# Kernel optimization log

Measured on AMD Instinct MI355X. Metric: run time of the kernel, lower is better.

Reference implementation:

```python
import jax, jax.numpy as jnp
import numpy as np

CHUNK = 32
FLOOR = 0.01
EPS_MIX = 1e-5
EPS_NORM = 1e-5


def l2norm(x):
    return x / jnp.sqrt(jnp.sum(x * x, -1, keepdims=True) + 1e-12)


def dw_causal_conv(x, w):
    # x: (B, L, C), w: (C, K) depthwise causal conv, tap K-1 is 'current'
    K = w.shape[-1]
    L = x.shape[1]
    xp = jnp.pad(x, ((0, 0), (K - 1, 0), (0, 0)))
    y = jnp.zeros_like(x)
    for t in range(K):
        y = y + xp[:, t:t + L, :] * w[:, t]
    return y


def delta_rule_chunkwise(q, k, v, beta):
    # q,k: (B,H,L,dk), v: (B,H,L,dv), beta: (B,H,L); L % CHUNK == 0
    b, h, L, dk = q.shape
    dv = v.shape[-1]
    c = CHUNK
    n = L // c
    q = l2norm(q)
    k = l2norm(k)
    v = v * beta[..., None]
    kb = k * beta[..., None]
    rs = lambda x: x.reshape(b, h, n, c, -1)
    qc, kc, vc, kbc = rs(q), rs(k), rs(v), rs(kb)
    # in-chunk inverse of (I + tril(K_beta K^T)) via forward substitution
    T = -jnp.einsum('bhnid,bhnjd->bhnij', kbc, kc)
    tri_strict = jnp.tril(jnp.ones((c, c), bool), -1)
    T = jnp.where(tri_strict, T, 0.0)
    for i in range(1, c):
        T = T.at[..., i, :i].add(
            jnp.einsum('bhnj,bhnji->bhni', T[..., i, :], T[..., :, :i]))
    T = T + jnp.eye(c, dtype=T.dtype)
    u = jnp.einsum('bhnij,bhnjd->bhnid', T, vc)
    w = jnp.einsum('bhnij,bhnjd->bhnid', T, kbc)
    mask_incl = jnp.tril(jnp.ones((c, c), bool), 0)

    def step(S, inp):
        qi, ki, ui, wi = inp  # each (b,h,c,d)
        attn = jnp.einsum('bhid,bhjd->bhij', qi, ki)
        attn = jnp.where(mask_incl, attn, 0.0)
        u_i = ui - jnp.einsum('bhik,bhkd->bhid', wi, S)
        o_i = jnp.einsum('bhik,bhkd->bhid', qi, S) + jnp.einsum('bhij,bhjd->bhid', attn, u_i)
        S = S + jnp.einsum('bhci,bhcd->bhid', ki, u_i)
        return S, o_i

    S0 = jnp.zeros((b, h, dk, dv), q.dtype)
    xs = tuple(jnp.moveaxis(a, 2, 0) for a in (qc, kc, u, w))
    S, o = jax.lax.scan(step, S0, xs)
    o = jnp.moveaxis(o, 0, 2).reshape(b, h, L, dv)
    return o, S


def setup_inputs() -> dict:
    key = jax.random.key(0)
    B, L, D, H = 4, 4096, 1024, 4
    dh = D // H  # 256
    ks = jax.random.split(key, 20)
    s = 1.0 / np.sqrt(D)
    inp = {
        'hidden_states': jax.random.normal(ks[0], (B, L, D), jnp.float32),
        'Wq': jax.random.normal(ks[1], (D, D), jnp.float32) * s,
        'Wk': jax.random.normal(ks[2], (D, D), jnp.float32) * s,
        'Wv': jax.random.normal(ks[3], (D, D), jnp.float32) * s,
        'Wb': jax.random.normal(ks[4], (D, H), jnp.float32) * s,
        'conv_q_w': jax.random.normal(ks[5], (D, 4), jnp.float32) * 0.5,
        'conv_k_w': jax.random.normal(ks[6], (D, 4), jnp.float32) * 0.5,
        'conv_v_w': jax.random.normal(ks[7], (D, 4), jnp.float32) * 0.5,
        'local_w': (jax.random.normal(ks[8], (H * dh, 7), jnp.float32) / np.sqrt(7.0)).at[:, -1].add(1.0),
        'mid_w': (jax.random.normal(ks[9], (H * dh, 25), jnp.float32) / np.sqrt(25.0)).at[:, -1].add(1.0),
        'r_w1': jax.random.normal(ks[10], (D + 14 * H, 2 * (D + 14 * H)), jnp.float32) / np.sqrt(D + 14 * H),
        'r_b1': jnp.zeros((2 * (D + 14 * H),), jnp.float32),
        'r_w2': jax.random.normal(ks[11], (2 * (D + 14 * H), H * 4), jnp.float32) / np.sqrt(2.0 * (D + 14 * H)),
        'r_b2': jnp.zeros((H, 4), jnp.float32).at[:, 2:].set(0.7).reshape(-1),
        'mix_w': jnp.ones((H, dh), jnp.float32),
        'onorm_w': jnp.ones((dh,), jnp.float32),
        'Wo': jax.random.normal(ks[12], (D, D), jnp.float32) * s,
    }
    return inp


def reference(hidden_states, Wq, Wk, Wv, Wb, conv_q_w, conv_k_w, conv_v_w,
              local_w, mid_w, r_w1, r_b1, r_w2, r_b2, mix_w, onorm_w, Wo):
    B, L, D = hidden_states.shape
    H = mix_w.shape[0]
    dh = mix_w.shape[1]
    # projections + short causal depthwise convs with SiLU (qk_activation='silu')
    q = jax.nn.silu(dw_causal_conv(hidden_states @ Wq, conv_q_w))
    k = jax.nn.silu(dw_causal_conv(hidden_states @ Wk, conv_k_w))
    v = jax.nn.silu(dw_causal_conv(hidden_states @ Wv, conv_v_w))
    q4 = q.reshape(B, L, H, dh)
    k4 = k.reshape(B, L, H, dh)
    v4 = v.reshape(B, L, H, dh)
    beta = jax.nn.sigmoid(hidden_states @ Wb)  # (B,L,H)
    delta_out, _ = delta_rule_chunkwise(
        jnp.transpose(q4, (0, 2, 1, 3)), jnp.transpose(k4, (0, 2, 1, 3)),
        jnp.transpose(v4, (0, 2, 1, 3)), jnp.transpose(beta, (0, 2, 1)))
    delta_out = jnp.transpose(delta_out, (0, 2, 1, 3))  # (B,L,H,dh)
    v_direct = v4
    vflat = v4.reshape(B, L, H * dh)
    local_out = dw_causal_conv(vflat, local_w).reshape(B, L, H, dh)
    mid_out = dw_causal_conv(vflat, mid_w).reshape(B, L, H, dh)
    outs = [local_out, mid_out, delta_out, v_direct]
    # router stats: per-head mean/var of each path + pairwise mean dots
    feats = []
    for o_ in outs:
        feats.append(o_.mean(-1))
        feats.append(jnp.var(o_, -1, ddof=1))
    for i in range(4):
        for j in range(i + 1, 4):
            feats.append((outs[i] * outs[j]).mean(-1))
    router_feat = jnp.concatenate([hidden_states] + feats, axis=-1)  # (B,L,D+14H)
    h1 = jax.nn.silu(router_feat @ r_w1 + r_b1)
    logits = (h1 @ r_w2 + r_b2).reshape(B, L, H, 4)
    p = jax.nn.softmax(logits, -1)
    p = p * (1.0 - 4.0 * FLOOR) + FLOOR  # probability floor
    mixed = sum(p[..., i:i + 1] * outs[i] for i in range(4))  # (B,L,H,dh)
    # MixNorm: per-token per-head RMSNorm with (H,dh) affine
    rms = jnp.sqrt(jnp.mean(mixed * mixed, -1, keepdims=True) + EPS_MIX)
    mixed = mixed / rms * mix_w
    # output RMSNorm (per head_v_dim)
    rms2 = jnp.sqrt(jnp.mean(mixed * mixed, -1, keepdims=True) + EPS_NORM)
    o_n = mixed / rms2 * onorm_w
    return o_n.reshape(B, L, H * dh) @ Wo
```

## Files before the change

### kernel.cpp

```cpp
#include <hip/hip_runtime.h>
#include <cstdint>
#include <cstddef>

typedef unsigned short u16;
typedef __bf16 bf16x8 __attribute__((ext_vector_type(8)));
typedef float    f32x4 __attribute__((ext_vector_type(4)));
typedef unsigned short u16x8 __attribute__((ext_vector_type(8)));
typedef unsigned short u16x4 __attribute__((ext_vector_type(4)));

#define MFMA16(a,b,c) __builtin_amdgcn_mfma_f32_16x16x32_bf16(a,b,c,0,0,0)

__device__ __forceinline__ float bf2f(u16 u){ return __uint_as_float(((unsigned)u)<<16); }
__device__ __forceinline__ u16 f2bf(float f){
  unsigned x = __float_as_uint(f);
  unsigned r = x + 0x7fffu + ((x>>16)&1u);
  return (u16)(r>>16);
}
__device__ __forceinline__ float wred(float v){
  #pragma unroll
  for (int o=32;o;o>>=1) v += __shfl_xor(v,o,64);
  return v;
}
__device__ __forceinline__ float siluf(float x){ return x/(1.f+__expf(-x)); }

__global__ __launch_bounds__(256) void k_zero(float* __restrict__ p, int n){
  int i = blockIdx.x*256 + threadIdx.x;
  if (i < n) p[i] = 0.f;
}

__global__ __launch_bounds__(256) void k_cvt(const float* __restrict__ src,
                                             u16* __restrict__ dst, int n){
  int i = (blockIdx.x*256 + threadIdx.x)*4;
  if (i < n){
    float4 f = *(const float4*)(src + i);
    u16x4 o; o[0]=f2bf(f.x); o[1]=f2bf(f.y); o[2]=f2bf(f.z); o[3]=f2bf(f.w);
    *(u16x4*)(dst + i) = o;
  }
}

__global__ __launch_bounds__(256) void k_tr(const float* __restrict__ src, u16* __restrict__ dst,
                                            int R, int C, int Rp, int Cp){
  __shared__ float t[32][33];
  int n0 = blockIdx.x*32, k0 = blockIdx.y*32;
  int tx = threadIdx.x & 31, ty = threadIdx.x >> 5;
  #pragma unroll
  for (int j=0;j<4;j++){
    int k = k0 + ty + j*8, nn = n0 + tx;
    t[ty + j*8][tx] = (k < R && nn < C) ? src[k*C + nn] : 0.f;
  }
  __syncthreads();
  #pragma unroll
  for (int j=0;j<4;j++){
    int nn = n0 + ty + j*8, k = k0 + tx;
    dst[nn*Rp + k] = f2bf(t[tx][ty + j*8]);
  }
}

__global__ __launch_bounds__(256) void k_pad_w2t(const float* __restrict__ src, u16* __restrict__ dst){
  int k = blockIdx.x*256 + threadIdx.x;
  int j = blockIdx.y;
  if (k < 2176) dst[j*2176 + k] = (k < 2160) ? f2bf(src[k*16 + j]) : (u16)0;
}
__global__ __launch_bounds__(256) void k_pad_b1(const float* __restrict__ src, float* __restrict__ dst){
  int i = blockIdx.x*256 + threadIdx.x;
  if (i < 2176) dst[i] = (i<2160) ? src[i] : 0.f;
}

__global__ __launch_bounds__(256) void k_trk(const u16* __restrict__ kn, u16* __restrict__ kTb){
  __shared__ u16 vs[32][264];
  const int g = blockIdx.x;
  const int bh = g >> 7, nc = g & 127;
  const int b = bh >> 2, h = bh & 3;
  const int tid = threadIdx.x;
  const int rr = tid >> 3, cb = (tid & 7) * 32;
  const u16* src = kn + (size_t)(b*4096 + nc*32 + rr)*1024 + h*256 + cb;
  #pragma unroll
  for (int v=0; v<4; ++v){
    u16x8 x = *(const u16x8*)(src + v*8);
    *(u16x8*)&vs[rr][cb + v*8] = x;
  }
  __syncthreads();
  u16* dst = kTb + ((size_t)g*256 + tid)*32;
  #pragma unroll
  for (int v=0; v<4; ++v){
    u16x8 o;
    #pragma unroll
    for (int e=0; e<8; e++) o[e] = vs[v*8 + e][tid];
    *(u16x8*)(dst + v*8) = o;
  }
}

__global__ __launch_bounds__(256,2) void k_gemm(
    const u16* __restrict__ A, const u16* __restrict__ Bt, void* __restrict__ Cvp,
    int M, int N, int K, int out_f32)
{
  __shared__ u16 As[2][128*64];
  __shared__ u16 Bs[2][128*64];
  const int tid = threadIdx.x;
  const int lane = tid & 63, wv = tid >> 6;
  const int wm = (wv>>1)*64, wn = (wv&1)*64;
  const int r15 = lane & 15, q4 = lane >> 4;
  const int bm0 = blockIdx.y*128, bn0 = blockIdx.x*128;
  const int srow = tid>>3, sch = tid&7;
  const int nk = K >> 6;

  const f32x4 fz = {0.f,0.f,0.f,0.f};
  f32x4 acc[4][4];
  #pragma unroll
  for (int i=0;i<4;i++){
    #pragma unroll
    for (int j=0;j<4;j++) acc[i][j] = fz;
  }

  {
    u16x8 ca[4], cb[4];
    #pragma unroll
    for (int i=0;i<4;i++){
      int r = i*32 + srow;
      ca[i] = *(const u16x8*)(A  + (size_t)(bm0+r)*K + sch*8);
      cb[i] = *(const u16x8*)(Bt + (size_t)(bn0+r)*K + sch*8);
    }
    #pragma unroll
    for (int i=0;i<4;i++){
      int r = i*32 + srow;
      int byt = r*128 + ((sch ^ (r&7))*16);
      *(u16x8*)((char*)(&As[0][0]) + byt) = ca[i];
      *(u16x8*)((char*)(&Bs[0][0]) + byt) = cb[i];
    }
  }
  int cur = 0;
  for (int t=0; t<nk; ++t){
    u16x8 na[4], nb[4];
    if (t+1 < nk){
      const int kt = (t+1)<<6;
      #pragma unroll
      for (int i=0;i<4;i++){
        int r = i*32 + srow;
        na[i] = *(const u16x8*)(A  + (size_t)(bm0+r)*K + kt + sch*8);
        nb[i] = *(const u16x8*)(Bt + (size_t)(bn0+r)*K + kt + sch*8);
      }
    }
    __syncthreads();
    const u16* as_ = &As[cur][0];
    const u16* bs_ = &Bs[cur][0];
    #pragma unroll
    for (int kk=0; kk<2; ++kk){
      bf16x8 av[4], bv[4];
      #pragma unroll
      for (int mi=0;mi<4;mi++){
        int row = wm + mi*16 + r15;
        int ch  = kk*4 + q4;
        av[mi] = *(const bf16x8*)((const char*)as_ + row*128 + ((ch ^ (row&7))*16));
      }
      #pragma unroll
      for (int ni=0;ni<4;ni++){
        int row = wn + ni*16 + r15;
        int ch  = kk*4 + q4;
        bv[ni] = *(const bf16x8*)((const char*)bs_ + row*128 + ((ch ^ (row&7))*16));
      }
      #pragma unroll
      for (int mi=0;mi<4;mi++){
        #pragma unroll
        for (int ni=0;ni<4;ni++)
          acc[mi][ni] = MFMA16(av[mi], bv[ni], acc[mi][ni]);
      }
    }
    if (t+1 < nk){
      #pragma unroll
      for (int i=0;i<4;i++){
        int r = i*32 + srow;
        int byt = r*128 + ((sch ^ (r&7))*16);
        *(u16x8*)((char*)(&As[cur^1][0]) + byt) = na[i];
        *(u16x8*)((char*)(&Bs[cur^1][0]) + byt) = nb[i];
      }
    }
    cur ^= 1;
  }
  float* Cf = (float*)Cvp;
  u16*  Cb2 = (u16*)Cvp;
  #pragma unroll
  for (int mi=0;mi<4;mi++){
    #pragma unroll
    for (int ni=0;ni<4;ni++){
      int gr = bm0 + wm + mi*16 + q4*4;
      int gc = bn0 + wn + ni*16 + r15;
      #pragma unroll
      for (int rg=0; rg<4; ++rg){
        float v = acc[mi][ni][rg];
        size_t off = (size_t)(gr+rg)*N + gc;
        if (out_f32) Cf[off] = v; else Cb2[off] = f2bf(v);
      }
    }
  }
}

union SMu {
  struct { u16 As[2][128*64]; u16 Bs[2][128*64]; } g;
  u16 h1s[128][136];
};
__global__ __launch_bounds__(256,2) void k_gemm_router(
    const u16* __restrict__ A, const u16* __restrict__ Bt,
    const float* __restrict__ bias, const u16* __restrict__ w2t,
    float* __restrict__ logits)
{
  __shared__ SMu sm;
  const int tid = threadIdx.x;
  const int lane = tid & 63, wv = tid >> 6;
  const int wm = (wv>>1)*64, wn = (wv&1)*64;
  const int r15 = lane & 15, q4 = lane >> 4;
  const int bm0 = blockIdx.y*128, bn0 = blockIdx.x*128;
  const int srow = tid>>3, sch = tid&7;
  const int K = 1088, nk = 17;

  const f32x4 fz = {0.f,0.f,0.f,0.f};
  f32x4 acc[4][4];
  #pragma unroll
  for (int i=0;i<4;i++){
    #pragma unroll
    for (int j=0;j<4;j++) acc[i][j] = fz;
  }
  {
    u16x8 ca[4], cb[4];
    #pragma unroll
    for (int i=0;i<4;i++){
      int r = i*32 + srow;
      ca[i] = *(const u16x8*)(A  + (size_t)(bm0+r)*K + sch*8);
      cb[i] = *(const u16x8*)(Bt + (size_t)(bn0+r)*K + sch*8);
    }
    #pragma unroll
    for (int i=0;i<4;i++){
      int r = i*32 + srow;
      int byt = r*128 + ((sch ^ (r&7))*16);
      *(u16x8*)((char*)(&sm.g.As[0][0]) + byt) = ca[i];
      *(u16x8*)((char*)(&sm.g.Bs[0][0]) + byt) = cb[i];
    }
  }
  int cur = 0;
  for (int t=0; t<nk; ++t){
    u16x8 na[4], nb[4];
    if (t+1 < nk){
      const int kt = (t+1)<<6;
      #pragma unroll
      for (int i=0;i<4;i++){
        int r = i*32 + srow;
        na[i] = *(const u16x8*)(A  + (size_t)(bm0+r)*K + kt + sch*8);
        nb[i] = *(const u16x8*)(Bt + (size_t)(bn0+r)*K + kt + sch*8);
      }
    }
    __syncthreads();
    const u16* as_ = &sm.g.As[cur][0];
    const u16* bs_ = &sm.g.Bs[cur][0];
    #pragma unroll
    for (int kk=0; kk<2; ++kk){
      bf16x8 av[4], bv[4];
      #pragma unroll
      for (int mi=0;mi<4;mi++){
        int row = wm + mi*16 + r15;
        int ch  = kk*4 + q4;
        av[mi] = *(const bf16x8*)((const char*)as_ + row*128 + ((ch ^ (row&7))*16));
      }
      #pragma unroll
      for (int ni=0;ni<4;ni++){
        int row = wn + ni*16 + r15;
        int ch  = kk*4 + q4;
        bv[ni] = *(const bf16x8*)((const char*)bs_ + row*128 + ((ch ^ (row&7))*16));
      }
      #pragma unroll
      for (int mi=0;mi<4;mi++){
        #pragma unroll
        for (int ni=0;ni<4;ni++)
          acc[mi][ni] = MFMA16(av[mi], bv[ni], acc[mi][ni]);
      }
    }
    if (t+1 < nk){
      #pragma unroll
      for (int i=0;i<4;i++){
        int r = i*32 + srow;
        int byt = r*128 + ((sch ^ (r&7))*16);
        *(u16x8*)((char*)(&sm.g.As[cur^1][0]) + byt) = na[i];
        *(u16x8*)((char*)(&sm.g.Bs[cur^1][0]) + byt) = nb[i];
      }
    }
    cur ^= 1;
  }
  __syncthreads();
  #pragma unroll
  for (int mi=0;mi<4;mi++){
    #pragma unroll
    for (int ni=0;ni<4;ni++){
      int lr = wm + mi*16 + q4*4;
      int lc = wn + ni*16 + r15;
      float bv_ = bias[bn0 + lc];
      #pragma unroll
      for (int rg=0; rg<4; ++rg)
        sm.h1s[lr+rg][lc] = f2bf(siluf(acc[mi][ni][rg] + bv_));
    }
  }
  __syncthreads();
  f32x4 lacc[2] = {fz, fz};
  #pragma unroll
  for (int rt=0; rt<2; ++rt){
    #pragma unroll
    for (int ks=0; ks<4; ++ks){
      bf16x8 a = *(const bf16x8*)((const char*)&sm.h1s[wv*32 + rt*16 + r15][0] + ks*64 + q4*16);
      bf16x8 b = *(const bf16x8*)(w2t + r15*2176 + bn0 + ks*32 + q4*8);
      lacc[rt] = MFMA16(a, b, lacc[rt]);
    }
  }
  #pragma unroll
  for (int rt=0; rt<2; ++rt){
    #pragma unroll
    for (int rg=0; rg<4; ++rg){
      int m = bm0 + wv*32 + rt*16 + q4*4 + rg;
      atomicAdd(&logits[m*16 + r15], lacc[rt][rg]);
    }
  }
}

__global__ __launch_bounds__(256) void k_softm(float* __restrict__ p, const float* __restrict__ b2){
  int m = blockIdx.x*256 + threadIdx.x;
  float l[16];
  #pragma unroll
  for (int j=0;j<16;j++) l[j] = p[m*16+j] + b2[j];
  #pragma unroll
  for (int hh=0;hh<4;hh++){
    float l0=l[hh*4+0], l1=l[hh*4+1], l2=l[hh*4+2], l3=l[hh*4+3];
    float mx = fmaxf(fmaxf(l0,l1),fmaxf(l2,l3));
    float e0=__expf(l0-mx), e1=__expf(l1-mx), e2=__expf(l2-mx), e3=__expf(l3-mx);
    float iv = 1.f/(e0+e1+e2+e3);
    p[m*16+hh*4+0]=e0*iv*0.96f+0.01f;
    p[m*16+hh*4+1]=e1*iv*0.96f+0.01f;
    p[m*16+hh*4+2]=e2*iv*0.96f+0.01f;
    p[m*16+hh*4+3]=e3*iv*0.96f+0.01f;
  }
}

__global__ __launch_bounds__(256) void k_beta(const u16* __restrict__ Xb,
                                              const float* __restrict__ Wb,
                                              float* __restrict__ beta){
  int m = blockIdx.x*4 + (threadIdx.x>>6);
  int lane = threadIdx.x & 63;
  float a0=0.f,a1=0.f,a2=0.f,a3=0.f;
  #pragma unroll 4
  for (int i=0;i<16;i++){
    int k = lane + i*64;
    float x = bf2f(Xb[m*1024 + k]);
    float4 wr = *(const float4*)(Wb + k*4);
    a0 += x*wr.x; a1 += x*wr.y; a2 += x*wr.z; a3 += x*wr.w;
  }
  a0 = wred(a0); a1 = wred(a1); a2 = wred(a2); a3 = wred(a3);
  if (lane == 0){
    beta[m*4+0] = 1.f/(1.f+__expf(-a0));
    beta[m*4+1] = 1.f/(1.f+__expf(-a1));
    beta[m*4+2] = 1.f/(1.f+__expf(-a2));
    beta[m*4+3] = 1.f/(1.f+__expf(-a3));
  }
}

__global__ __launch_bounds__(256) void k_conv(const u16* __restrict__ raw,
                                              const float* __restrict__ cw,
                                              u16* __restrict__ outp, int do_norm){
  const int m = blockIdx.x;
  const int tid = threadIdx.x, lane = tid&63, hh = tid>>6;
  const int l = m & 4095;
  const int cbase = hh*256 + lane*4;
  float x[4][4];
  #pragma unroll
  for (int j=0;j<4;j++){
    if (l >= j){
      u16x4 xv = *(const u16x4*)(raw + (m-j)*1024 + cbase);
      #pragma unroll
      for (int e=0;e<4;e++) x[j][e] = bf2f(xv[e]);
    } else {
      #pragma unroll
      for (int e=0;e<4;e++) x[j][e] = 0.f;
    }
  }
  float y[4]; float ss = 0.f;
  #pragma unroll
  for (int e=0;e<4;e++){
    int c = cbase + e;
    float yy = x[0][e]*cw[c*4+3] + x[1][e]*cw[c*4+2] + x[2][e]*cw[c*4+1] + x[3][e]*cw[c*4+0];
    yy = siluf(yy);
    y[e] = yy; ss += yy*yy;
  }
  if (do_norm){
    ss = wred(ss);
    float sc = rsqrtf(ss + 1e-12f);
    #pragma unroll
    for (int e=0;e<4;e++) y[e] *= sc;
  }
  u16x4 o;
  #pragma unroll
  for (int e=0;e<4;e++) o[e] = f2bf(y[e]);
  *(u16x4*)(outp + m*1024 + cbase) = o;
}

__global__ __launch_bounds__(256) void k_localmid(const u16* __restrict__ v,
                                                  const float* __restrict__ lw,
                                                  const float* __restrict__ mw,
                                                  u16* __restrict__ lo, u16* __restrict__ mo){
  __shared__ u16 vs[56][256];
  const int lt0 = blockIdx.x*32;
  const int b = blockIdx.y;
  const int c0 = blockIdx.z*256;
  const int tid = threadIdx.x;
  #pragma unroll
  for (int i=0;i<7;i++){
    int flat = tid + i*256;
    int row = flat >> 5;
    int cc = (flat & 31)*8;
    int tok = lt0 - 24 + row;
    u16x8 val = {0,0,0,0,0,0,0,0};
    if (tok >= 0) val = *(const u16x8*)(v + (b*4096 + tok)*1024 + c0 + cc);
    *(u16x8*)&vs[row][cc] = val;
  }
  __syncthreads();
  const int c = tid;
  float lwr[7], mwr[25];
  #pragma unroll
  for (int i=0;i<7;i++) lwr[i] = lw[(c0+c)*7 + i];
  #pragma unroll
  for (int i=0;i<25;i++) mwr[i] = mw[(c0+c)*25 + i];
  for (int lt=0; lt<32; ++lt){
    float a7=0.f, a25=0.f;
    #pragma unroll
    for (int t=0;t<25;t++) a25 += bf2f(vs[lt+t][c]) * mwr[t];
    #pragma unroll
    for (int t=0;t<7;t++)  a7  += bf2f(vs[18+lt+t][c]) * lwr[t];
    int m = b*4096 + lt0 + lt;
    lo[m*1024 + c0 + c] = f2bf(a7);
    mo[m*1024 + c0 + c] = f2bf(a25);
  }
}

__global__ __launch_bounds__(256,2) void k_chunk(
    const u16* __restrict__ qn, const u16* __restrict__ kn, const u16* __restrict__ v,
    const float* __restrict__ beta, u16* __restrict__ u_, u16* __restrict__ w_,
    u16* __restrict__ attnb)
{
  const int chk = blockIdx.x;
  const int nc = chk & 127;
  const int bh = chk >> 7;
  const int b = bh >> 2, h = bh & 3;
  const int tok0 = b*4096 + nc*32;
  const int tid = threadIdx.x, lane = tid&63, wv = tid>>6;
  const int r15 = lane&15, q4 = lane>>4;

  __shared__ u16 kbT[256][40];
  __shared__ u16 vbT[256][40];
  __shared__ float Tm[4][32][33];
  __shared__ u16 Xs[32][40];

  {
    int rr = tid >> 3;
    int cb = (tid & 7)*32;
    float bt = beta[(tok0 + rr)*4 + h];
    const u16* ksrc = kn + (tok0+rr)*1024 + h*256 + cb;
    const u16* vsrc = v  + (tok0+rr)*1024 + h*256 + cb;
    #pragma unroll
    for (int vvv=0; vvv<4; ++vvv){
      u16x8 kx = *(const u16x8*)(ksrc + vvv*8);
      u16x8 vx = *(const u16x8*)(vsrc + vvv*8);
      #pragma unroll
      for (int e=0;e<8;e++){
        kbT[cb + vvv*8 + e][rr] = f2bf(bf2f(kx[e]) * bt);
        vbT[cb + vvv*8 + e][rr] = f2bf(bf2f(vx[e]) * bt);
      }
    }
  }
  {
    const int i0 = (wv>>1)*16, j0 = (wv&1)*16;
    float bi = beta[(tok0 + i0 + r15)*4 + h];
    f32x4 tacc = {0.f,0.f,0.f,0.f};
    #pragma unroll
    for (int ks=0; ks<8; ++ks){
      u16x8 ar = *(const u16x8*)(kn + (tok0 + i0 + r15)*1024 + h*256 + ks*32 + q4*8);
      union { u16x8 u; bf16x8 bf; } au;
      #pragma unroll
      for (int e=0;e<8;e++) au.u[e] = f2bf(bf2f(ar[e]) * bi);
      bf16x8 bv = *(const bf16x8*)(kn + (tok0 + j0 + r15)*1024 + h*256 + ks*32 + q4*8);
      tacc = MFMA16(au.bf, bv, tacc);
    }
    #pragma unroll
    for (int rg=0; rg<4; ++rg){
      int i = i0 + q4*4 + rg, j = j0 + r15;
      float val = (i > j) ? -tacc[rg] : 0.f;
      Tm[0][i][j] = val;
      Tm[2][i][j] = val + ((i==j)?1.f:0.f);
    }
  }
  __syncthreads();
  int cbuf = 0, cx = 2;
  const int ii = tid >> 3, jj = (tid&7)*4;
  for (int s=0; s<4; ++s){
    int nb = cbuf^1, nx = cx^1;
    {
      float o0=0.f,o1=0.f,o2=0.f,o3=0.f;
      for (int k=0;k<32;k++){
        float a = Tm[cbuf][ii][k];
        o0 += a*Tm[cbuf][k][jj+0]; o1 += a*Tm[cbuf][k][jj+1];
        o2 += a*Tm[cbuf][k][jj+2]; o3 += a*Tm[cbuf][k][jj+3];
      }
      Tm[nb][ii][jj+0]=o0; Tm[nb][ii][jj+1]=o1; Tm[nb][ii][jj+2]=o2; Tm[nb][ii][jj+3]=o3;
    }
    __syncthreads();
    {
      float o0=Tm[cx][ii][jj+0], o1=Tm[cx][ii][jj+1], o2=Tm[cx][ii][jj+2], o3=Tm[cx][ii][jj+3];
      for (int k=0;k<32;k++){
        float a = Tm[nb][ii][k];
        o0 += a*Tm[cx][k][jj+0]; o1 += a*Tm[cx][k][jj+1];
        o2 += a*Tm[cx][k][jj+2]; o3 += a*Tm[cx][k][jj+3];
      }
      Tm[nx][ii][jj+0]=o0; Tm[nx][ii][jj+1]=o1; Tm[nx][ii][jj+2]=o2; Tm[nx][ii][jj+3]=o3;
    }
    __syncthreads();
    cbuf = nb; cx = nx;
  }
  {
    #pragma unroll
    for (int e=0;e<4;e++) Xs[ii][jj+e] = f2bf(Tm[cx][ii][jj+e]);
  }
  __syncthreads();
  {
    #pragma unroll
    for (int nt=0; nt<4; ++nt){
      int n0 = wv*64 + nt*16;
      #pragma unroll
      for (int mt=0; mt<2; ++mt){
        bf16x8 a = *(const bf16x8*)((const char*)&Xs[mt*16 + r15][0] + q4*16);
        bf16x8 bu = *(const bf16x8*)((const char*)&vbT[n0 + r15][0] + q4*16);
        bf16x8 bw = *(const bf16x8*)((const char*)&kbT[n0 + r15][0] + q4*16);
        f32x4 ua = {0.f,0.f,0.f,0.f};
        f32x4 wa = {0.f,0.f,0.f,0.f};
        ua = MFMA16(a, bu, ua);
        wa = MFMA16(a, bw, wa);
        #pragma unroll
        for (int rg=0;rg<4;rg++){
          int row = mt*16 + q4*4 + rg;
          int col = n0 + r15;
          u_[(chk*32 + row)*256 + col] = f2bf(ua[rg]);
          w_[(chk*32 + row)*256 + col] = f2bf(wa[rg]);
        }
      }
    }
  }
  {
    const int i0 = (wv>>1)*16, j0 = (wv&1)*16;
    f32x4 aacc = {0.f,0.f,0.f,0.f};
    #pragma unroll
    for (int ks=0;ks<8;++ks){
      bf16x8 a = *(const bf16x8*)(qn + (tok0 + i0 + r15)*1024 + h*256 + ks*32 + q4*8);
      bf16x8 bv = *(const bf16x8*)(kn + (tok0 + j0 + r15)*1024 + h*256 + ks*32 + q4*8);
      aacc = MFMA16(a, bv, aacc);
    }
    #pragma unroll
    for (int rg=0;rg<4;rg++){
      int i = i0 + q4*4 + rg, j = j0 + r15;
      attnb[chk*1024 + i*32 + j] = f2bf((i>=j)? aacc[rg] : 0.f);
    }
  }
}

#define SCAN_BODY(NC, WCUR, WNXT, CB, NB) { \
  const int chk_ = bh*128 + (NC); \
  const int ncn_ = ((NC)+1 < 128) ? (NC)+1 : 127; \
  const int chkn_ = bh*128 + ncn_; \
  u16x8 kst[4]; \
  { const u16* kc = kTb + (size_t)chkn_*8192 + tid*32; \
    _Pragma("unroll") for (int v=0;v<4;++v) kst[v] = *(const u16x8*)(kc + v*8); } \
  _Pragma("unroll") for (int ks=0;ks<8;++ks) \
    WNXT[ks] = *(const u16x8*)(w_ + (size_t)(chkn_*32 + tm*16 + r15)*256 + ks*32 + q4*8); \
  u16x8 qv[8]; \
  _Pragma("unroll") for (int ks=0;ks<8;++ks) \
    qv[ks] = *(const u16x8*)(qn + (size_t)(b*4096 + (NC)*32 + tm*16 + r15)*1024 + h*256 + ks*32 + q4*8); \
  u16x8 atv = *(const u16x8*)(attnb + (size_t)chk_*1024 + (tm*16 + r15)*32 + q4*8); \
  u16 uvv[4]; \
  _Pragma("unroll") for (int rg=0;rg<4;++rg) \
    uvv[rg] = u_[(size_t)(chk_*32 + tm*16 + q4*4 + rg)*256 + dv0 + tn*16 + r15]; \
  f32x4 ua = fz, ub2 = fz; \
  _Pragma("unroll") for (int ks=0;ks<8;ks+=2){ \
    bf16x8 s0 = *(const bf16x8*)((const char*)&Sb[CB][tn*16 + r15][0] + ks*64 + q4*16); \
    ua = MFMA16(*(const bf16x8*)&WCUR[ks], s0, ua); \
    bf16x8 s1 = *(const bf16x8*)((const char*)&Sb[CB][tn*16 + r15][0] + (ks+1)*64 + q4*16); \
    ub2 = MFMA16(*(const bf16x8*)&WCUR[ks+1], s1, ub2); } \
  _Pragma("unroll") for (int rg=0;rg<4;++rg){ \
    float uiv = bf2f(uvv[rg]) - ua[rg] - ub2[rg]; \
    uT[tn*16 + r15][tm*16 + q4*4 + rg] = f2bf(uiv); } \
  __syncthreads(); \
  f32x4 oa = fz, ob = fz; \
  _Pragma("unroll") for (int ks=0;ks<8;ks+=2){ \
    bf16x8 s0 = *(const bf16x8*)((const char*)&Sb[CB][tn*16 + r15][0] + ks*64 + q4*16); \
    oa = MFMA16(*(const bf16x8*)&qv[ks], s0, oa); \
    bf16x8 s1 = *(const bf16x8*)((const char*)&Sb[CB][tn*16 + r15][0] + (ks+1)*64 + q4*16); \
    ob = MFMA16(*(const bf16x8*)&qv[ks+1], s1, ob); } \
  { bf16x8 bu = *(const bf16x8*)((const char*)&uT[tn*16 + r15][0] + q4*16); \
    oa = MFMA16(*(const bf16x8*)&atv, bu, oa); } \
  _Pragma("unroll") for (int rg=0;rg<4;++rg) \
    od[(size_t)(b*4096 + (NC)*32 + tm*16 + q4*4 + rg)*1024 + h*256 + dv0 + tn*16 + r15] = f2bf(oa[rg] + ob[rg]); \
  _Pragma("unroll") for (int mt=0;mt<4;++mt){ \
    bf16x8 a = *(const bf16x8*)((const char*)&knT[CB][wv*64 + mt*16 + r15][0] + q4*16); \
    _Pragma("unroll") for (int ntl=0;ntl<2;++ntl){ \
      bf16x8 bu = *(const bf16x8*)((const char*)&uT[ntl*16 + r15][0] + q4*16); \
      Sacc[mt][ntl] = MFMA16(a, bu, Sacc[mt][ntl]); } } \
  _Pragma("unroll") for (int mt=0;mt<4;++mt) \
    _Pragma("unroll") for (int ntl=0;ntl<2;++ntl) \
      _Pragma("unroll") for (int rg=0;rg<4;++rg) \
        Sb[NB][ntl*16 + r15][wv*64 + mt*16 + q4*4 + rg] = f2bf(Sacc[mt][ntl][rg]); \
  _Pragma("unroll") for (int v=0;v<4;++v) *(u16x8*)(&knT[NB][tid][0] + v*8) = kst[v]; \
  __syncthreads(); }

__global__ __launch_bounds__(256,1) void k_scan(
    const u16* __restrict__ qn, const u16* __restrict__ kTb,
    const u16* __restrict__ u_, const u16* __restrict__ w_,
    const u16* __restrict__ attnb, u16* __restrict__ od)
{
  const int bid = blockIdx.x;
  const int bh = bid >> 3;
  const int b = bh >> 2, h = bh & 3;
  const int dv0 = (bid & 7)*32;
  const int tid = threadIdx.x, lane = tid & 63, wv = tid >> 6;
  const int tm = wv >> 1, tn = wv & 1;
  const int r15 = lane & 15, q4 = lane >> 4;

  __shared__ u16 Sb[2][32][264];
  __shared__ u16 knT[2][256][36];
  __shared__ u16 uT[32][36];

  for (int i = tid; i < 32*264; i += 256) (&Sb[0][0][0])[i] = 0;
  const f32x4 fz = {0.f,0.f,0.f,0.f};
  f32x4 Sacc[4][2];
  #pragma unroll
  for (int a_=0;a_<4;a_++){
    #pragma unroll
    for (int b_=0;b_<2;b_++) Sacc[a_][b_] = fz;
  }
  {
    const u16* kc = kTb + (size_t)(bh*128)*8192 + tid*32;
    u16x8 k0[4];
    #pragma unroll
    for (int v=0;v<4;++v) k0[v] = *(const u16x8*)(kc + v*8);
    #pragma unroll
    for (int v=0;v<4;++v) *(u16x8*)(&knT[0][tid][0] + v*8) = k0[v];
  }
  u16x8 wA[8], wB[8];
  #pragma unroll
  for (int ks=0;ks<8;++ks)
    wA[ks] = *(const u16x8*)(w_ + (size_t)((bh*128)*32 + tm*16 + r15)*256 + ks*32 + q4*8);
  __syncthreads();

  for (int nc = 0; nc < 128; nc += 2){
    SCAN_BODY(nc,   wA, wB, 0, 1)
    SCAN_BODY(nc+1, wB, wA, 1, 0)
  }
}

__global__ __launch_bounds__(256) void k_feats(
    const float* __restrict__ Xf, const u16* __restrict__ lo, const u16* __restrict__ mo,
    const u16* __restrict__ de, const u16* __restrict__ vv, u16* __restrict__ feat)
{
  const int m = blockIdx.x;
  const int tid = threadIdx.x, lane = tid & 63, hh = tid >> 6;
  {
    float4 xv = *(const float4*)(Xf + m*1024 + tid*4);
    u16x4 o; o[0]=f2bf(xv.x); o[1]=f2bf(xv.y); o[2]=f2bf(xv.z); o[3]=f2bf(xv.w);
    *(u16x4*)(feat + m*1088 + tid*4) = o;
  }
  if (tid < 8) feat[m*1088 + 1080 + tid] = 0;
  const int base = m*1024 + hh*256 + lane*4;
  u16x4 a0 = *(const u16x4*)(lo + base);
  u16x4 a1 = *(const u16x4*)(mo + base);
  u16x4 a2 = *(const u16x4*)(de + base);
  u16x4 a3 = *(const u16x4*)(vv + base);
  float s[14];
  #pragma unroll
  for (int i=0;i<14;i++) s[i]=0.f;
  #pragma unroll
  for (int e=0;e<4;e++){
    float L = bf2f(a0[e]), Mm = bf2f(a1[e]), D = bf2f(a2[e]), V = bf2f(a3[e]);
    s[0]+=L; s[1]+=L*L; s[2]+=Mm; s[3]+=Mm*Mm; s[4]+=D; s[5]+=D*D; s[6]+=V; s[7]+=V*V;
    s[8]+=L*Mm; s[9]+=L*D; s[10]+=L*V; s[11]+=Mm*D; s[12]+=Mm*V; s[13]+=D*V;
  }
  #pragma unroll
  for (int i=0;i<14;i++) s[i] = wred(s[i]);
  if (lane == 0){
    const float inv = 1.f/256.f, invv = 1.f/255.f;
    u16* fb = feat + m*1088 + 1024;
    float mn[4] = {s[0]*inv, s[2]*inv, s[4]*inv, s[6]*inv};
    float vr[4] = {(s[1]-256.f*mn[0]*mn[0])*invv, (s[3]-256.f*mn[1]*mn[1])*invv,
                   (s[5]-256.f*mn[2]*mn[2])*invv, (s[7]-256.f*mn[3]*mn[3])*invv};
    #pragma unroll
    for (int i=0;i<4;i++){ fb[(2*i)*4 + hh] = f2bf(mn[i]); fb[(2*i+1)*4 + hh] = f2bf(vr[i]); }
    #pragma unroll
    for (int i=0;i<6;i++) fb[(8+i)*4 + hh] = f2bf(s[8+i]*inv);
  }
}

__global__ __launch_bounds__(256) void k_mix(
    const u16* __restrict__ lo, const u16* __restrict__ mo, const u16* __restrict__ de,
    const u16* __restrict__ vv, const float* __restrict__ p,
    const float* __restrict__ mixw, const float* __restrict__ onw, u16* __restrict__ on)
{
  const int m = blockIdx.x;
  const int tid = threadIdx.x, lane = tid&63, hh = tid>>6;
  const int dbase = lane*4;
  const int base = m*1024 + hh*256 + dbase;
  float4 pv = *(const float4*)(p + m*16 + hh*4);
  u16x4 a0 = *(const u16x4*)(lo + base);
  u16x4 a1 = *(const u16x4*)(mo + base);
  u16x4 a2 = *(const u16x4*)(de + base);
  u16x4 a3 = *(const u16x4*)(vv + base);
  float g[4]; float ss = 0.f;
  #pragma unroll
  for (int e=0;e<4;e++){
    float x = pv.x*bf2f(a0[e]) + pv.y*bf2f(a1[e]) + pv.z*bf2f(a2[e]) + pv.w*bf2f(a3[e]);
    g[e]=x; ss += x*x;
  }
  ss = wred(ss);
  float r1 = rsqrtf(ss*(1.f/256.f) + 1e-5f);
  float ss2 = 0.f;
  #pragma unroll
  for (int e=0;e<4;e++){ g[e] = g[e]*r1*mixw[hh*256 + dbase + e]; ss2 += g[e]*g[e]; }
  ss2 = wred(ss2);
  float r2 = rsqrtf(ss2*(1.f/256.f) + 1e-5f);
  u16x4 o;
  #pragma unroll
  for (int e=0;e<4;e++) o[e] = f2bf(g[e]*r2*onw[dbase + e]);
  *(u16x4*)(on + base) = o;
}

extern "C" void kernel_launch(void* const* d_in, const int* in_sizes, int n_in,
                              void* d_out, int out_size, void* d_ws, size_t ws_size,
                              hipStream_t stream)
{
  const float* X   = (const float*)d_in[0];
  const float* Wq  = (const float*)d_in[1];
  const float* Wk  = (const float*)d_in[2];
  const float* Wv  = (const float*)d_in[3];
  const float* Wb  = (const float*)d_in[4];
  const float* cqw = (const float*)d_in[5];
  const float* ckw = (const float*)d_in[6];
  const float* cvw = (const float*)d_in[7];
  const float* lw  = (const float*)d_in[8];
  const float* mw  = (const float*)d_in[9];
  const float* rw1 = (const float*)d_in[10];
  const float* rb1 = (const float*)d_in[11];
  const float* rw2 = (const float*)d_in[12];
  const float* rb2 = (const float*)d_in[13];
  const float* mixw= (const float*)d_in[14];
  const float* onw = (const float*)d_in[15];
  const float* Wo  = (const float*)d_in[16];

  char* ws = (char*)d_ws;
  const size_t SLOT = 33554432;
  char* s0 = ws;
  char* s1 = ws + 1*SLOT;
  char* s2 = ws + 2*SLOT;
  char* s3 = ws + 3*SLOT;
  char* s4 = ws + 4*SLOT;
  char* s5 = ws + 5*SLOT;
  char* s6 = ws + 6*SLOT;
  char* ext = ws + 7*SLOT;
  u16*   attb  = (u16*)(ext);
  float* pb    = (float*)(ext + 4194304);
  float* betab = (float*)(ext + 4194304 + 1048576);
  char*  wsp   = ext + 4194304 + 1048576 + 262144;
  u16* Wqt = (u16*)(wsp);
  u16* Wkt = (u16*)(wsp + 2097152);
  u16* Wvt = (u16*)(wsp + 2*2097152);
  u16* Wot = (u16*)(wsp + 3*2097152);
  u16* w1t = (u16*)(wsp + 4*2097152);
  u16* w2t = (u16*)(wsp + 4*2097152 + 4734976);
  float* b1p = (float*)(wsp + 4*2097152 + 4734976 + 69632);

  u16* Xb    = (u16*)s0;
  u16* rawb  = (u16*)s1;
  u16* qnb   = (u16*)s2;
  u16* knb   = (u16*)s3;
  u16* vpb   = (u16*)s4;
  u16* ub    = (u16*)s0;
  u16* wbuf  = (u16*)s1;
  u16* odb   = (u16*)s5;
  u16* kTbp  = (u16*)s6;
  u16* lob   = (u16*)s2;
  u16* mob   = (u16*)s3;
  u16* featb = (u16*)s0;
  u16* onb   = (u16*)s0;

  k_zero<<<1024,256,0,stream>>>(pb, 262144);
  k_cvt<<<16384,256,0,stream>>>(X, Xb, 16777216);
  k_tr<<<dim3(32,32),256,0,stream>>>(Wq, Wqt, 1024,1024,1024,1024);
  k_tr<<<dim3(32,32),256,0,stream>>>(Wk, Wkt, 1024,1024,1024,1024);
  k_tr<<<dim3(32,32),256,0,stream>>>(Wv, Wvt, 1024,1024,1024,1024);
  k_tr<<<dim3(32,32),256,0,stream>>>(Wo, Wot, 1024,1024,1024,1024);
  k_tr<<<dim3(68,34),256,0,stream>>>(rw1, w1t, 1080,2160,1088,2176);
  k_pad_w2t<<<dim3(9,16),256,0,stream>>>(rw2, w2t);
  k_pad_b1<<<9,256,0,stream>>>(rb1, b1p);
  k_gemm<<<dim3(8,128),256,0,stream>>>(Xb, Wqt, rawb, 16384,1024,1024, 0);
  k_conv<<<16384,256,0,stream>>>(rawb, cqw, qnb, 1);
  k_gemm<<<dim3(8,128),256,0,stream>>>(Xb, Wkt, rawb, 16384,1024,1024, 0);
  k_conv<<<16384,256,0,stream>>>(rawb, ckw, knb, 1);
  k_gemm<<<dim3(8,128),256,0,stream>>>(Xb, Wvt, rawb, 16384,1024,1024, 0);
  k_conv<<<16384,256,0,stream>>>(rawb, cvw, vpb, 0);
  k_beta<<<4096,256,0,stream>>>(Xb, Wb, betab);
  k_chunk<<<2048,256,0,stream>>>(qnb, knb, vpb, betab, ub, wbuf, attb);
  k_trk<<<2048,256,0,stream>>>(knb, kTbp);
  k_scan<<<128,256,0,stream>>>(qnb, kTbp, ub, wbuf, attb, odb);
  k_localmid<<<dim3(128,4,4),256,0,stream>>>(vpb, lw, mw, lob, mob);
  k_feats<<<16384,256,0,stream>>>(X, lob, mob, odb, vpb, featb);
  k_gemm_router<<<dim3(17,128),256,0,stream>>>(featb, w1t, b1p, w2t, pb);
  k_softm<<<64,256,0,stream>>>(pb, rb2);
  k_mix<<<16384,256,0,stream>>>(lob, mob, odb, vpb, pb, mixw, onw, onb);
  k_gemm<<<dim3(8,128),256,0,stream>>>(onb, Wot, d_out, 16384,1024,1024, 1);
}
```

Before: 1.250 ms.

## Prefetch scan operands into registers and drop the kT shared-memory staging

The chunk-scan kernel now loads the next chunk's k fragments, w, attn and u values straight into registers one iteration ahead, through a double-buffered context struct. This removes the knT shared-memory staging buffer and its store/load round trip. S fragments are read from LDS once and reused for both the u and o products, LDS stores are packed into 4-wide writes, and barriers are replaced by lgkmcnt-only waits plus s_barrier so outstanding global loads are not drained. Block-to-(bh,dv) mapping is also permuted so neighbouring blocks cover different heads. In exchange, register pressure rises.

```diff
diff --git a/kernel.cpp b/kernel.cpp
--- a/kernel.cpp
+++ b/kernel.cpp
@@ -562,53 +562,58 @@
   }
 }
 
-#define SCAN_BODY(NC, WCUR, WNXT, CB, NB) { \
-  const int chk_ = bh*128 + (NC); \
-  const int ncn_ = ((NC)+1 < 128) ? (NC)+1 : 127; \
-  const int chkn_ = bh*128 + ncn_; \
-  u16x8 kst[4]; \
-  { const u16* kc = kTb + (size_t)chkn_*8192 + tid*32; \
-    _Pragma("unroll") for (int v=0;v<4;++v) kst[v] = *(const u16x8*)(kc + v*8); } \
+struct ScanCtx { u16x8 kf[4]; u16x8 wf[8]; u16x8 at; u16 uv[4]; };
+
+#define SBAR() do{ asm volatile("s_waitcnt lgkmcnt(0)" ::: "memory"); \
+                   __builtin_amdgcn_s_barrier(); \
+                   asm volatile("" ::: "memory"); }while(0)
+
+#define SPREF(C, CHK) { \
+  const u16* kp = kTb + ((size_t)(CHK)*256 + wv*64 + r15)*32 + q4*8; \
+  _Pragma("unroll") for (int mt=0;mt<4;++mt) C.kf[mt] = *(const u16x8*)(kp + mt*512); \
+  const u16* wp = w_ + ((size_t)(CHK)*32 + tm*16 + r15)*256 + q4*8; \
+  _Pragma("unroll") for (int ks=0;ks<8;++ks) C.wf[ks] = *(const u16x8*)(wp + ks*32); \
+  C.at = *(const u16x8*)(attnb + (size_t)(CHK)*1024 + (tm*16 + r15)*32 + q4*8); \
+  const u16* up = u_ + ((size_t)(CHK)*32 + tm*16 + q4*4)*256 + dv0 + tn*16 + r15; \
+  _Pragma("unroll") for (int rg=0;rg<4;++rg) C.uv[rg] = up[rg*256]; \
+}
+
+#define SBODY(C, N, NC, CB, NB) { \
+  const int chkn_ = chkbase + (((NC)+1 < 128) ? (NC)+1 : 127); \
+  SPREF(N, chkn_); \
+  u16x8 qf[8]; \
+  { const u16* qp = qn + (size_t)(tokbase + (NC)*32 + tm*16 + r15)*1024 + h*256 + q4*8; \
+    _Pragma("unroll") for (int ks=0;ks<8;++ks) qf[ks] = *(const u16x8*)(qp + ks*32); } \
+  bf16x8 sf[8]; \
   _Pragma("unroll") for (int ks=0;ks<8;++ks) \
-    WNXT[ks] = *(const u16x8*)(w_ + (size_t)(chkn_*32 + tm*16 + r15)*256 + ks*32 + q4*8); \
-  u16x8 qv[8]; \
-  _Pragma("unroll") for (int ks=0;ks<8;++ks) \
-    qv[ks] = *(const u16x8*)(qn + (size_t)(b*4096 + (NC)*32 + tm*16 + r15)*1024 + h*256 + ks*32 + q4*8); \
-  u16x8 atv = *(const u16x8*)(attnb + (size_t)chk_*1024 + (tm*16 + r15)*32 + q4*8); \
-  u16 uvv[4]; \
-  _Pragma("unroll") for (int rg=0;rg<4;++rg) \
-    uvv[rg] = u_[(size_t)(chk_*32 + tm*16 + q4*4 + rg)*256 + dv0 + tn*16 + r15]; \
-  f32x4 ua = fz, ub2 = fz; \
+    sf[ks] = *(const bf16x8*)((const char*)&Sb[CB][tn*16 + r15][0] + ks*64 + q4*16); \
+  f32x4 ua = fz, ub = fz; \
   _Pragma("unroll") for (int ks=0;ks<8;ks+=2){ \
-    bf16x8 s0 = *(const bf16x8*)((const char*)&Sb[CB][tn*16 + r15][0] + ks*64 + q4*16); \
-    ua = MFMA16(*(const bf16x8*)&WCUR[ks], s0, ua); \
-    bf16x8 s1 = *(const bf16x8*)((const char*)&Sb[CB][tn*16 + r15][0] + (ks+1)*64 + q4*16); \
-    ub2 = MFMA16(*(const bf16x8*)&WCUR[ks+1], s1, ub2); } \
-  _Pragma("unroll") for (int rg=0;rg<4;++rg){ \
-    float uiv = bf2f(uvv[rg]) - ua[rg] - ub2[rg]; \
-    uT[tn*16 + r15][tm*16 + q4*4 + rg] = f2bf(uiv); } \
-  __syncthreads(); \
+    ua = MFMA16(*(const bf16x8*)&C.wf[ks],   sf[ks],   ua); \
+    ub = MFMA16(*(const bf16x8*)&C.wf[ks+1], sf[ks+1], ub); } \
+  { u16x4 pk; \
+    _Pragma("unroll") for (int rg=0;rg<4;++rg) pk[rg] = f2bf(bf2f(C.uv[rg]) - ua[rg] - ub[rg]); \
+    *(u16x4*)&uT[tn*16 + r15][tm*16 + q4*4] = pk; } \
+  SBAR(); \
+  bf16x8 bu0 = *(const bf16x8*)((const char*)&uT[r15][0] + q4*16); \
+  bf16x8 bu1 = *(const bf16x8*)((const char*)&uT[16 + r15][0] + q4*16); \
   f32x4 oa = fz, ob = fz; \
   _Pragma("unroll") for (int ks=0;ks<8;ks+=2){ \
-    bf16x8 s0 = *(const bf16x8*)((const char*)&Sb[CB][tn*16 + r15][0] + ks*64 + q4*16); \
-    oa = MFMA16(*(const bf16x8*)&qv[ks], s0, oa); \
-    bf16x8 s1 = *(const bf16x8*)((const char*)&Sb[CB][tn*16 + r15][0] + (ks+1)*64 + q4*16); \
-    ob = MFMA16(*(const bf16x8*)&qv[ks+1], s1, ob); } \
-  { bf16x8 bu = *(const bf16x8*)((const char*)&uT[tn*16 + r15][0] + q4*16); \
-    oa = MFMA16(*(const bf16x8*)&atv, bu, oa); } \
+    oa = MFMA16(*(const bf16x8*)&qf[ks],   sf[ks],   oa); \
+    ob = MFMA16(*(const bf16x8*)&qf[ks+1], sf[ks+1], ob); } \
+  oa = MFMA16(*(const bf16x8*)&C.at, (tn ? bu1 : bu0), oa); \
   _Pragma("unroll") for (int rg=0;rg<4;++rg) \
-    od[(size_t)(b*4096 + (NC)*32 + tm*16 + q4*4 + rg)*1024 + h*256 + dv0 + tn*16 + r15] = f2bf(oa[rg] + ob[rg]); \
+    od[(size_t)(tokbase + (NC)*32 + tm*16 + q4*4 + rg)*1024 + h*256 + dv0 + tn*16 + r15] = f2bf(oa[rg] + ob[rg]); \
   _Pragma("unroll") for (int mt=0;mt<4;++mt){ \
-    bf16x8 a = *(const bf16x8*)((const char*)&knT[CB][wv*64 + mt*16 + r15][0] + q4*16); \
+    Sacc[mt][0] = MFMA16(*(const bf16x8*)&C.kf[mt], bu0, Sacc[mt][0]); \
+    Sacc[mt][1] = MFMA16(*(const bf16x8*)&C.kf[mt], bu1, Sacc[mt][1]); } \
+  _Pragma("unroll") for (int mt=0;mt<4;++mt){ \
     _Pragma("unroll") for (int ntl=0;ntl<2;++ntl){ \
-      bf16x8 bu = *(const bf16x8*)((const char*)&uT[ntl*16 + r15][0] + q4*16); \
-      Sacc[mt][ntl] = MFMA16(a, bu, Sacc[mt][ntl]); } } \
-  _Pragma("unroll") for (int mt=0;mt<4;++mt) \
-    _Pragma("unroll") for (int ntl=0;ntl<2;++ntl) \
-      _Pragma("unroll") for (int rg=0;rg<4;++rg) \
-        Sb[NB][ntl*16 + r15][wv*64 + mt*16 + q4*4 + rg] = f2bf(Sacc[mt][ntl][rg]); \
-  _Pragma("unroll") for (int v=0;v<4;++v) *(u16x8*)(&knT[NB][tid][0] + v*8) = kst[v]; \
-  __syncthreads(); }
+      u16x4 pk; \
+      _Pragma("unroll") for (int rg=0;rg<4;++rg) pk[rg] = f2bf(Sacc[mt][ntl][rg]); \
+      *(u16x4*)&Sb[NB][ntl*16 + r15][wv*64 + mt*16 + q4*4] = pk; } } \
+  SBAR(); \
+}
 
 __global__ __launch_bounds__(256,1) void k_scan(
     const u16* __restrict__ qn, const u16* __restrict__ kTb,
@@ -616,18 +621,19 @@
     const u16* __restrict__ attnb, u16* __restrict__ od)
 {
   const int bid = blockIdx.x;
-  const int bh = bid >> 3;
+  const int bh  = (bid & 7) | (((bid >> 3) & 1) << 3);
+  const int dv0 = (bid >> 4) * 32;
   const int b = bh >> 2, h = bh & 3;
-  const int dv0 = (bid & 7)*32;
   const int tid = threadIdx.x, lane = tid & 63, wv = tid >> 6;
   const int tm = wv >> 1, tn = wv & 1;
   const int r15 = lane & 15, q4 = lane >> 4;
+  const int chkbase = bh * 128;
+  const int tokbase = b * 4096;
 
   __shared__ u16 Sb[2][32][264];
-  __shared__ u16 knT[2][256][36];
-  __shared__ u16 uT[32][36];
-
-  for (int i = tid; i < 32*264; i += 256) (&Sb[0][0][0])[i] = 0;
+  __shared__ u16 uT[32][40];
+
+  for (int i = tid; i < 2*32*264; i += 256) (&Sb[0][0][0])[i] = 0;
   const f32x4 fz = {0.f,0.f,0.f,0.f};
   f32x4 Sacc[4][2];
   #pragma unroll
@@ -635,23 +641,13 @@
     #pragma unroll
     for (int b_=0;b_<2;b_++) Sacc[a_][b_] = fz;
   }
-  {
-    const u16* kc = kTb + (size_t)(bh*128)*8192 + tid*32;
-    u16x8 k0[4];
-    #pragma unroll
-    for (int v=0;v<4;++v) k0[v] = *(const u16x8*)(kc + v*8);
-    #pragma unroll
-    for (int v=0;v<4;++v) *(u16x8*)(&knT[0][tid][0] + v*8) = k0[v];
-  }
-  u16x8 wA[8], wB[8];
-  #pragma unroll
-  for (int ks=0;ks<8;++ks)
-    wA[ks] = *(const u16x8*)(w_ + (size_t)((bh*128)*32 + tm*16 + r15)*256 + ks*32 + q4*8);
+  ScanCtx cA, cB;
+  SPREF(cA, chkbase);
   __syncthreads();
 
   for (int nc = 0; nc < 128; nc += 2){
-    SCAN_BODY(nc,   wA, wB, 0, 1)
-    SCAN_BODY(nc+1, wB, wA, 1, 0)
+    SBODY(cA, cB, nc,   0, 1)
+    SBODY(cB, cA, nc+1, 1, 0)
   }
 }
 
```

Measured after the change: 1.149 ms. 8.1% less time.
